# Optimization experiments

Measured on AMD Instinct MI355X. Metric: run time of the kernel, lower is better.

Reference implementation:

```python
import jax, jax.numpy as jnp
import numpy as np

B, L, E, H, A = 32, 4096, 512, 512, 256


def setup_inputs() -> dict:
    key = jax.random.key(0)
    ks = jax.random.split(key, 8)
    s_e = 1.0 / np.sqrt(E)
    s_h = 1.0 / np.sqrt(H)
    s_a = 1.0 / np.sqrt(A)
    return {
        "features": jax.random.normal(ks[0], (B, L, E), jnp.float32),
        "decoder_hidden": jax.random.normal(ks[1], (B, H), jnp.float32),
        "W_enc": jax.random.uniform(ks[2], (E, A), jnp.float32, -s_e, s_e),
        "b_enc": jax.random.uniform(ks[3], (A,), jnp.float32, -s_e, s_e),
        "W_dec": jax.random.uniform(ks[4], (H, A), jnp.float32, -s_h, s_h),
        "b_dec": jax.random.uniform(ks[5], (A,), jnp.float32, -s_h, s_h),
        "W_v": jax.random.uniform(ks[6], (A, 1), jnp.float32, -s_a, s_a),
        "b_v": jax.random.uniform(ks[7], (1,), jnp.float32, -s_a, s_a),
    }


def reference(features, decoder_hidden, W_enc, b_enc, W_dec, b_dec, W_v, b_v):
    # encoder/decoder projections
    enc_attn = jnp.einsum("ble,ea->bla", features, W_enc) + b_enc  # [B,L,A]
    dec_attn = decoder_hidden @ W_dec + b_dec                       # [B,A]
    sim = jax.nn.relu(enc_attn + dec_attn[:, None, :])              # [B,L,A]
    scores = (jnp.einsum("bla,ao->blo", sim, W_v) + b_v)[..., 0]    # [B,L]
    attn_weights = jax.nn.softmax(scores, axis=1)                   # [B,L]
    output = jnp.einsum("ble,bl->be", features, attn_weights)       # [B,E]
    return output, attn_weights
```

## Files before the change

### kernel.cpp

```cpp
#include <hip/hip_runtime.h>
#include <hip/hip_bf16.h>
#include <stdint.h>


typedef __attribute__((ext_vector_type(8))) short bf16x8;
typedef __attribute__((ext_vector_type(4))) float f32x4;

__device__ __forceinline__ unsigned short f32_to_bf16(float f) {
    union { float f; unsigned u; } v; v.f = f;
    unsigned u = v.u;
    u += 0x7fffu + ((u >> 16) & 1u);
    return (unsigned short)(u >> 16);
}

__device__ __forceinline__ void async_load16(const void* g, void* l) {
    __builtin_amdgcn_global_load_lds(
        (const __attribute__((address_space(1))) unsigned int*)g,
        (__attribute__((address_space(3))) unsigned int*)l, 16, 0, 0);
}

__global__ __launch_bounds__(256) void prep_kernel(
    const float* __restrict__ dh, const float* __restrict__ W_enc,
    const float* __restrict__ b_enc, const float* __restrict__ W_dec,
    const float* __restrict__ b_dec, unsigned short* __restrict__ Wp,
    float* __restrict__ dec_full)
{
    int t = threadIdx.x;
    if (blockIdx.x < 32) {
        int b = blockIdx.x;
        float acc = b_enc[t] + b_dec[t];
        for (int h = 0; h < 512; ++h)
            acc += dh[b * 512 + h] * W_dec[h * 256 + t];
        dec_full[b * 256 + t] = acc;
    } else {
        int tid = (blockIdx.x - 32) * 256 + t;
        #pragma unroll
        for (int i = 0; i < 8; ++i) {
            int d = tid + i * 16384;
            int j = d & 7;
            int n = (d >> 3) & 255;
            int chunk = (d >> 11) & 7;
            int kb = d >> 14;
            int k = kb * 64 + chunk * 8 + j;
            Wp[d] = f32_to_bf16(W_enc[k * 256 + n]);
        }
    }
}

__global__ __launch_bounds__(256) void score_kernel(
    const float* __restrict__ feat, const unsigned short* __restrict__ Wp,
    const float* __restrict__ dec_full, const float* __restrict__ W_v,
    float* __restrict__ scores)
{
    __shared__ unsigned short Alds[8192];
    __shared__ unsigned short Blds[16384];
    __shared__ float red[4][128];

    const int t = threadIdx.x;
    const int lane = t & 63;
    const int wave = t >> 6;
    const int r0 = blockIdx.x * 128;
    const int b = r0 >> 12;

    float wv[4], dec[4];
    #pragma unroll
    for (int ct = 0; ct < 4; ++ct) {
        int a = wave * 64 + ct * 16 + (lane & 15);
        wv[ct] = W_v[a];
        dec[ct] = dec_full[b * 256 + a];
    }

    f32x4 acc[8][4];
    #pragma unroll
    for (int mt = 0; mt < 8; ++mt)
        #pragma unroll
        for (int ct = 0; ct < 4; ++ct)
            acc[mt][ct] = f32x4{0.f, 0.f, 0.f, 0.f};

    for (int ks = 0; ks < 8; ++ks) {
        #pragma unroll
        for (int q = 0; q < 8; ++q) {
            int c = q * 256 + wave * 64 + lane;
            async_load16(Wp + ks * 16384 + c * 8, Blds + c * 8);
        }
        float4 av[8];
        #pragma unroll
        for (int it = 0; it < 8; ++it) {
            int lin = it * 256 + t;
            int m = lin >> 4, kq = lin & 15;
            av[it] = *(const float4*)(feat + (size_t)(r0 + m) * 512 + ks * 64 + kq * 4);
        }
        #pragma unroll
        for (int it = 0; it < 8; ++it) {
            int lin = it * 256 + t;
            int m = lin >> 4, kq = lin & 15;
            int chunk = kq >> 1, jh = kq & 1;
            ushort4 w;
            w.x = f32_to_bf16(av[it].x);
            w.y = f32_to_bf16(av[it].y);
            w.z = f32_to_bf16(av[it].z);
            w.w = f32_to_bf16(av[it].w);
            int off = m * 64 + ((chunk ^ (m & 7)) * 8) + jh * 4;
            *(ushort4*)(Alds + off) = w;
        }
        __syncthreads();

        #pragma unroll
        for (int kk = 0; kk < 2; ++kk) {
            int chunk = kk * 4 + (lane >> 4);
            bf16x8 bfr[4];
            #pragma unroll
            for (int ct = 0; ct < 4; ++ct) {
                int n = wave * 64 + ct * 16 + (lane & 15);
                bfr[ct] = *(const bf16x8*)(Blds + (chunk * 256 + n) * 8);
            }
            #pragma unroll
            for (int mt = 0; mt < 8; ++mt) {
                int m = mt * 16 + (lane & 15);
                bf16x8 afr = *(const bf16x8*)(Alds + m * 64 + ((chunk ^ (m & 7)) * 8));
                #pragma unroll
                for (int ct = 0; ct < 4; ++ct)
                    acc[mt][ct] = __builtin_amdgcn_mfma_f32_16x16x32_bf16(
                        afr, bfr[ct], acc[mt][ct], 0, 0, 0);
            }
        }
        __syncthreads();
    }

    #pragma unroll
    for (int mt = 0; mt < 8; ++mt) {
        #pragma unroll
        for (int r = 0; r < 4; ++r) {
            float p = 0.f;
            #pragma unroll
            for (int ct = 0; ct < 4; ++ct) {
                float v = acc[mt][ct][r] + dec[ct];
                v = v > 0.f ? v : 0.f;
                p += v * wv[ct];
            }
            p += __shfl_xor(p, 1);
            p += __shfl_xor(p, 2);
            p += __shfl_xor(p, 4);
            p += __shfl_xor(p, 8);
            if ((lane & 15) == 0)
                red[wave][mt * 16 + (lane >> 4) * 4 + r] = p;
        }
    }
    __syncthreads();
    if (t < 128)
        scores[r0 + t] = red[0][t] + red[1][t] + red[2][t] + red[3][t];
}

__global__ __launch_bounds__(256) void softmax_kernel(
    const float* __restrict__ scores, float* __restrict__ out)
{
    __shared__ float sred[4];
    __shared__ float zred[4];
    int b = blockIdx.x, t = threadIdx.x;

    out[b * 512 + t] = 0.f;
    out[b * 512 + 256 + t] = 0.f;

    const float* s = scores + b * 4096;
    float vals[16];
    float m = -1e30f;
    #pragma unroll
    for (int i = 0; i < 16; ++i) { vals[i] = s[t + i * 256]; m = fmaxf(m, vals[i]); }
    #pragma unroll
    for (int o = 1; o < 64; o <<= 1) m = fmaxf(m, __shfl_xor(m, o));
    if ((t & 63) == 0) sred[t >> 6] = m;
    __syncthreads();
    m = fmaxf(fmaxf(sred[0], sred[1]), fmaxf(sred[2], sred[3]));

    float z = 0.f;
    #pragma unroll
    for (int i = 0; i < 16; ++i) { vals[i] = __expf(vals[i] - m); z += vals[i]; }
    #pragma unroll
    for (int o = 1; o < 64; o <<= 1) z += __shfl_xor(z, o);
    if ((t & 63) == 0) zred[t >> 6] = z;
    __syncthreads();
    z = zred[0] + zred[1] + zred[2] + zred[3];
    float inv = 1.f / z;
    #pragma unroll
    for (int i = 0; i < 16; ++i)
        out[16384 + b * 4096 + t + i * 256] = vals[i] * inv;
}

__global__ __launch_bounds__(256) void wsum_kernel(
    const float* __restrict__ feat, const float* __restrict__ outw,
    float* __restrict__ out)
{
    __shared__ float4 red2[128];
    int blk = blockIdx.x;
    int b = blk >> 4, lc = blk & 15;
    int t = threadIdx.x;
    int e4 = t & 127, lh = t >> 7;
    const float* w = outw + 16384 + b * 4096 + lc * 256;

    float4 acc = {0.f, 0.f, 0.f, 0.f};
    for (int i = 0; i < 128; ++i) {
        int l = i * 2 + lh;
        float wl = w[l];
        const float4 f = *(const float4*)(feat + (size_t)(b * 4096 + lc * 256 + l) * 512 + e4 * 4);
        acc.x += wl * f.x; acc.y += wl * f.y; acc.z += wl * f.z; acc.w += wl * f.w;
    }
    if (lh == 1) red2[e4] = acc;
    __syncthreads();
    if (lh == 0) {
        float4 o = red2[e4];
        atomicAdd(&out[b * 512 + e4 * 4 + 0], acc.x + o.x);
        atomicAdd(&out[b * 512 + e4 * 4 + 1], acc.y + o.y);
        atomicAdd(&out[b * 512 + e4 * 4 + 2], acc.z + o.z);
        atomicAdd(&out[b * 512 + e4 * 4 + 3], acc.w + o.w);
    }
}

extern "C" void kernel_launch(void* const* d_in, const int* in_sizes, int n_in,
                              void* d_out, int out_size, void* d_ws, size_t ws_size,
                              hipStream_t stream) {
    const float* feat  = (const float*)d_in[0];
    const float* dh    = (const float*)d_in[1];
    const float* W_enc = (const float*)d_in[2];
    const float* b_enc = (const float*)d_in[3];
    const float* W_dec = (const float*)d_in[4];
    const float* b_dec = (const float*)d_in[5];
    const float* W_v   = (const float*)d_in[6];

    unsigned short* Wp = (unsigned short*)d_ws;
    float* dec_full = (float*)((char*)d_ws + 262144);
    float* scores   = (float*)((char*)d_ws + 294912);
    float* out      = (float*)d_out;

    prep_kernel<<<96, 256, 0, stream>>>(dh, W_enc, b_enc, W_dec, b_dec, Wp, dec_full);
    score_kernel<<<1024, 256, 0, stream>>>(feat, Wp, dec_full, W_v, scores);
    softmax_kernel<<<32, 256, 0, stream>>>(scores, out);
    wsum_kernel<<<512, 256, 0, stream>>>(feat, out, out);
}
```

Measured before the change: 483.5 us.

## Fuse weighted feature sum into score kernel with flash-style partial softmax combine

The score kernel now computes a per-block local max and exponentiated weights, then accumulates a partial weighted sum of its 128 feature rows while they are likely still cache-resident. A small combine kernel rescales these partials using the global max and sum from the softmax kernel. This removes the separate wsum pass, which re-read all features, and its atomics. It also prefetches the next feature tile into registers during the MFMA loop, adds a launch_bounds occupancy hint, and splits the dec projection across four accumulators. The cost is extra register pressure and a small partial-output buffer in the workspace.

```diff
diff --git a/kernel.cpp b/kernel.cpp
--- a/kernel.cpp
+++ b/kernel.cpp
@@ -28,10 +28,15 @@
     int t = threadIdx.x;
     if (blockIdx.x < 32) {
         int b = blockIdx.x;
-        float acc = b_enc[t] + b_dec[t];
-        for (int h = 0; h < 512; ++h)
-            acc += dh[b * 512 + h] * W_dec[h * 256 + t];
-        dec_full[b * 256 + t] = acc;
+        float a0 = 0.f, a1 = 0.f, a2 = 0.f, a3 = 0.f;
+        #pragma unroll 2
+        for (int h = 0; h < 512; h += 4) {
+            a0 += dh[b * 512 + h + 0] * W_dec[(h + 0) * 256 + t];
+            a1 += dh[b * 512 + h + 1] * W_dec[(h + 1) * 256 + t];
+            a2 += dh[b * 512 + h + 2] * W_dec[(h + 2) * 256 + t];
+            a3 += dh[b * 512 + h + 3] * W_dec[(h + 3) * 256 + t];
+        }
+        dec_full[b * 256 + t] = (a0 + a1) + (a2 + a3) + b_enc[t] + b_dec[t];
     } else {
         int tid = (blockIdx.x - 32) * 256 + t;
         #pragma unroll
@@ -47,14 +52,19 @@
     }
 }
 
-__global__ __launch_bounds__(256) void score_kernel(
+__global__ __launch_bounds__(256, 2) void score_kernel(
     const float* __restrict__ feat, const unsigned short* __restrict__ Wp,
     const float* __restrict__ dec_full, const float* __restrict__ W_v,
-    float* __restrict__ scores)
+    float* __restrict__ scores, float* __restrict__ m_c,
+    float* __restrict__ o_part)
 {
     __shared__ unsigned short Alds[8192];
     __shared__ unsigned short Blds[16384];
     __shared__ float red[4][128];
+    __shared__ float sblk[128];
+    __shared__ float wexp[128];
+    __shared__ float mshr;
+    __shared__ float red2x[128], red2y[128], red2z[128], red2w[128];
 
     const int t = threadIdx.x;
     const int lane = t & 63;
@@ -77,34 +87,41 @@
         for (int ct = 0; ct < 4; ++ct)
             acc[mt][ct] = f32x4{0.f, 0.f, 0.f, 0.f};
 
+    float4 av[8];
+    #pragma unroll
+    for (int it = 0; it < 8; ++it) {
+        int lin = it * 256 + t;
+        int m = lin >> 4, kq = lin & 15;
+        av[it] = *(const float4*)(feat + (size_t)(r0 + m) * 512 + kq * 4);
+    }
+
     for (int ks = 0; ks < 8; ++ks) {
         #pragma unroll
         for (int q = 0; q < 8; ++q) {
             int c = q * 256 + wave * 64 + lane;
             async_load16(Wp + ks * 16384 + c * 8, Blds + c * 8);
         }
-        float4 av[8];
         #pragma unroll
         for (int it = 0; it < 8; ++it) {
             int lin = it * 256 + t;
             int m = lin >> 4, kq = lin & 15;
-            av[it] = *(const float4*)(feat + (size_t)(r0 + m) * 512 + ks * 64 + kq * 4);
-        }
-        #pragma unroll
-        for (int it = 0; it < 8; ++it) {
-            int lin = it * 256 + t;
-            int m = lin >> 4, kq = lin & 15;
-            int chunk = kq >> 1, jh = kq & 1;
             ushort4 w;
             w.x = f32_to_bf16(av[it].x);
             w.y = f32_to_bf16(av[it].y);
             w.z = f32_to_bf16(av[it].z);
             w.w = f32_to_bf16(av[it].w);
-            int off = m * 64 + ((chunk ^ (m & 7)) * 8) + jh * 4;
-            *(ushort4*)(Alds + off) = w;
+            int chunk = kq >> 1, jh = kq & 1;
+            *(ushort4*)(Alds + m * 64 + ((chunk ^ (m & 7)) * 8) + jh * 4) = w;
         }
         __syncthreads();
-
+        if (ks < 7) {
+            #pragma unroll
+            for (int it = 0; it < 8; ++it) {
+                int lin = it * 256 + t;
+                int m = lin >> 4, kq = lin & 15;
+                av[it] = *(const float4*)(feat + (size_t)(r0 + m) * 512 + (ks + 1) * 64 + kq * 4);
+            }
+        }
         #pragma unroll
         for (int kk = 0; kk < 2; ++kk) {
             int chunk = kk * 4 + (lane >> 4);
@@ -147,20 +164,51 @@
         }
     }
     __syncthreads();
-    if (t < 128)
-        scores[r0 + t] = red[0][t] + red[1][t] + red[2][t] + red[3][t];
+    if (t < 128) {
+        float v = red[0][t] + red[1][t] + red[2][t] + red[3][t];
+        sblk[t] = v;
+        scores[r0 + t] = v;
+    }
+    __syncthreads();
+    if (t < 64) {
+        float m = fmaxf(sblk[t], sblk[t + 64]);
+        #pragma unroll
+        for (int o = 1; o < 64; o <<= 1) m = fmaxf(m, __shfl_xor(m, o));
+        if (t == 0) mshr = m;
+    }
+    __syncthreads();
+    float mb = mshr;
+    if (t < 128) wexp[t] = __expf(sblk[t] - mb);
+    __syncthreads();
+
+    int e4 = t & 127, lh = t >> 7;
+    float ax = 0.f, ay = 0.f, az = 0.f, aw = 0.f;
+    #pragma unroll 8
+    for (int i = 0; i < 64; ++i) {
+        int l = i * 2 + lh;
+        float wl = wexp[l];
+        const float4 f = *(const float4*)(feat + (size_t)(r0 + l) * 512 + e4 * 4);
+        ax += wl * f.x; ay += wl * f.y; az += wl * f.z; aw += wl * f.w;
+    }
+    if (lh) { red2x[e4] = ax; red2y[e4] = ay; red2z[e4] = az; red2w[e4] = aw; }
+    __syncthreads();
+    if (!lh) {
+        float4 r;
+        r.x = ax + red2x[e4]; r.y = ay + red2y[e4];
+        r.z = az + red2z[e4]; r.w = aw + red2w[e4];
+        *(float4*)(o_part + (size_t)blockIdx.x * 512 + e4 * 4) = r;
+        if (t == 0) m_c[blockIdx.x] = mb;
+    }
 }
 
 __global__ __launch_bounds__(256) void softmax_kernel(
-    const float* __restrict__ scores, float* __restrict__ out)
+    const float* __restrict__ scores, float* __restrict__ out,
+    float* __restrict__ MZ)
 {
     __shared__ float sred[4];
     __shared__ float zred[4];
     int b = blockIdx.x, t = threadIdx.x;
 
-    out[b * 512 + t] = 0.f;
-    out[b * 512 + 256 + t] = 0.f;
-
     const float* s = scores + b * 4096;
     float vals[16];
     float m = -1e30f;
@@ -184,35 +232,25 @@
     #pragma unroll
     for (int i = 0; i < 16; ++i)
         out[16384 + b * 4096 + t + i * 256] = vals[i] * inv;
-}
-
-__global__ __launch_bounds__(256) void wsum_kernel(
-    const float* __restrict__ feat, const float* __restrict__ outw,
-    float* __restrict__ out)
-{
-    __shared__ float4 red2[128];
-    int blk = blockIdx.x;
-    int b = blk >> 4, lc = blk & 15;
-    int t = threadIdx.x;
-    int e4 = t & 127, lh = t >> 7;
-    const float* w = outw + 16384 + b * 4096 + lc * 256;
-
-    float4 acc = {0.f, 0.f, 0.f, 0.f};
-    for (int i = 0; i < 128; ++i) {
-        int l = i * 2 + lh;
-        float wl = w[l];
-        const float4 f = *(const float4*)(feat + (size_t)(b * 4096 + lc * 256 + l) * 512 + e4 * 4);
-        acc.x += wl * f.x; acc.y += wl * f.y; acc.z += wl * f.z; acc.w += wl * f.w;
-    }
-    if (lh == 1) red2[e4] = acc;
-    __syncthreads();
-    if (lh == 0) {
-        float4 o = red2[e4];
-        atomicAdd(&out[b * 512 + e4 * 4 + 0], acc.x + o.x);
-        atomicAdd(&out[b * 512 + e4 * 4 + 1], acc.y + o.y);
-        atomicAdd(&out[b * 512 + e4 * 4 + 2], acc.z + o.z);
-        atomicAdd(&out[b * 512 + e4 * 4 + 3], acc.w + o.w);
-    }
+    if (t == 0) { MZ[b] = m; MZ[32 + b] = z; }
+}
+
+__global__ __launch_bounds__(256) void combine_kernel(
+    const float* __restrict__ o_part, const float* __restrict__ m_c,
+    const float* __restrict__ MZ, float* __restrict__ out)
+{
+    __shared__ float sc[32];
+    int b = blockIdx.x, t = threadIdx.x;
+    if (t < 32) sc[t] = __expf(m_c[b * 32 + t] - MZ[b]) * (1.f / MZ[32 + b]);
+    __syncthreads();
+    float a0 = 0.f, a1 = 0.f;
+    #pragma unroll 8
+    for (int c = 0; c < 32; ++c) {
+        const float2 v = *(const float2*)(o_part + (size_t)(b * 32 + c) * 512 + t * 2);
+        a0 += sc[c] * v.x; a1 += sc[c] * v.y;
+    }
+    float2 r; r.x = a0; r.y = a1;
+    *(float2*)(out + b * 512 + t * 2) = r;
 }
 
 extern "C" void kernel_launch(void* const* d_in, const int* in_sizes, int n_in,
@@ -229,10 +267,13 @@
     unsigned short* Wp = (unsigned short*)d_ws;
     float* dec_full = (float*)((char*)d_ws + 262144);
     float* scores   = (float*)((char*)d_ws + 294912);
+    float* m_c      = (float*)((char*)d_ws + 819200);
+    float* MZ       = (float*)((char*)d_ws + 823296);
+    float* o_part   = (float*)((char*)d_ws + 1048576);
     float* out      = (float*)d_out;
 
     prep_kernel<<<96, 256, 0, stream>>>(dh, W_enc, b_enc, W_dec, b_dec, Wp, dec_full);
-    score_kernel<<<1024, 256, 0, stream>>>(feat, Wp, dec_full, W_v, scores);
-    softmax_kernel<<<32, 256, 0, stream>>>(scores, out);
-    wsum_kernel<<<512, 256, 0, stream>>>(feat, out, out);
-}
+    score_kernel<<<1024, 256, 0, stream>>>(feat, Wp, dec_full, W_v, scores, m_c, o_part);
+    softmax_kernel<<<32, 256, 0, stream>>>(scores, out, MZ);
+    combine_kernel<<<32, 256, 0, stream>>>(o_part, m_c, MZ, out);
+}
```

Result: faster. 448.0 us (-7.3%).
